# Kernel optimization log

Hardware: AMD Instinct MI355X
Metric: run time of the kernel (lower is better)

The kernel has to match this reference:

```python
import jax, jax.numpy as jnp
import numpy as np

N, IN_DIM, HID, HEADS, HOPS, NCLS, E = 20000, 1536, 256, 4, 3, 3, 320000
HD = HID // HEADS
EPS = 1e-5
NEG_SLOPE = 0.2


def layer_norm(x, g, b):
    mu = jnp.mean(x, axis=-1, keepdims=True)
    var = jnp.var(x, axis=-1, keepdims=True)
    return (x - mu) * jax.lax.rsqrt(var + EPS) * g + b


def gatv2(x, src, dst, Wl, bl, Wr, br, att, bias):
    # x: [N, HID]; src/dst: [E'] (self loops included)
    xl = (x @ Wl + bl).reshape(N, HEADS, HD)  # source transform
    xr = (x @ Wr + br).reshape(N, HEADS, HD)  # target transform
    e = jax.nn.leaky_relu(xl[src] + xr[dst], NEG_SLOPE)          # [E', H, D]
    logits = jnp.einsum('ehd,hd->eh', e, att)                     # [E', H]
    m = jax.ops.segment_max(logits, dst, num_segments=N)         # [N, H]
    ex = jnp.exp(logits - m[dst])
    denom = jax.ops.segment_sum(ex, dst, num_segments=N)
    alpha = ex / denom[dst]                                       # softmax per dst
    msg = xl[src] * alpha[:, :, None]                             # [E', H, D]
    out = jax.ops.segment_sum(msg, dst, num_segments=N)
    return out.reshape(N, HID) + bias


def setup_inputs() -> dict:
    key = jax.random.key(0)
    ks = jax.random.split(key, 20)
    s = lambda k, shp, sc: jax.random.normal(k, shp, jnp.float32) * sc
    return {
        'features': s(ks[0], (N, IN_DIM), 1.0),
        'edge_index': jax.random.randint(ks[1], (2, E), 0, N, jnp.int64),
        'proj_W': s(ks[2], (IN_DIM, HID), 0.02),
        'proj_b': jnp.zeros((HID,), jnp.float32),
        'n0_g': jnp.ones((HID,), jnp.float32),
        'n0_b': jnp.zeros((HID,), jnp.float32),
        'Wl': s(ks[3], (HOPS, HID, HID), 0.05),
        'bl': jnp.zeros((HOPS, HID), jnp.float32),
        'Wr': s(ks[4], (HOPS, HID, HID), 0.05),
        'br': jnp.zeros((HOPS, HID), jnp.float32),
        'att': s(ks[5], (HOPS, HEADS, HD), 0.1),
        'gbias': jnp.zeros((HOPS, HID), jnp.float32),
        'ln_g': jnp.ones((HOPS, HID), jnp.float32),
        'ln_b': jnp.zeros((HOPS, HID), jnp.float32),
        'h1_W': s(ks[6], (HID, HID), 0.05),
        'h1_b': jnp.zeros((HID,), jnp.float32),
        'h2_W': s(ks[7], (HID, NCLS), 0.05),
        'h2_b': jnp.zeros((NCLS,), jnp.float32),
    }


def reference(features, edge_index, proj_W, proj_b, n0_g, n0_b, Wl, bl, Wr, br,
              att, gbias, ln_g, ln_b, h1_W, h1_b, h2_W, h2_b):
    # add self loops (PyG GATv2Conv default)
    loop = jnp.arange(N, dtype=edge_index.dtype)
    src = jnp.concatenate([edge_index[0], loop])
    dst = jnp.concatenate([edge_index[1], loop])

    x = layer_norm(features @ proj_W + proj_b, n0_g, n0_b)
    for h in range(HOPS):
        g = gatv2(x, src, dst, Wl[h], bl[h], Wr[h], br[h], att[h], gbias[h])
        x = layer_norm(g + x, ln_g[h], ln_b[h])
    # head (dropout inactive at eval); torch GELU is exact erf form
    x = jax.nn.gelu(x @ h1_W + h1_b, approximate=False)
    return x @ h2_W + h2_b
```

## Files before the change

### kernel.cpp

```cpp
#include <hip/hip_runtime.h>
#include <hip/hip_bf16.h>
#include <math.h>

#define NN 20000
#define INDIM 1536
#define HID 256
#define NE 320000
#define NEDGE (NE + NN)
#define EPSV 1e-5f
#define NEG 0.2f

typedef unsigned short ushort_b;
typedef unsigned int uint32;
typedef __bf16 bf16x8 __attribute__((ext_vector_type(8)));
typedef float f32x4 __attribute__((ext_vector_type(4)));

#define AS1(p) ((const __attribute__((address_space(1))) void*)(p))
#define AS3(p) ((__attribute__((address_space(3))) void*)(p))

__device__ inline ushort_b f2bf(float x) {
  union { float f; uint32 u; } v; v.f = x;
  uint32 r = v.u + 0x7FFFu + ((v.u >> 16) & 1u);
  return (ushort_b)(r >> 16);
}
__device__ inline float bf2f(ushort_b h) {
  union { uint32 u; float f; } v; v.u = ((uint32)h) << 16;
  return v.f;
}
__device__ inline float u2f(uint32 u) {
  union { uint32 u; float f; } v; v.u = u; return v.f;
}
__device__ inline uint32 cvtpk_bf16(float a, float b) {
  uint32 r;
  asm("v_cvt_pk_bf16_f32 %0, %1, %2" : "=v"(r) : "v"(a), "v"(b));
  return r;
}
__device__ inline float4 ldbf4(const ushort_b* p) {
  ushort4 u = *(const ushort4*)p;
  float4 f;
  f.x = bf2f(u.x); f.y = bf2f(u.y); f.z = bf2f(u.z); f.w = bf2f(u.w);
  return f;
}

template<int OUTMODE>
__global__ __launch_bounds__(256, 3) void gemm_mfma(
    const float* __restrict__ Af,
    const ushort_b* __restrict__ Bt0, const ushort_b* __restrict__ Bt1,
    const float* __restrict__ bias0, const float* __restrict__ bias1,
    void* __restrict__ C0, void* __restrict__ C1,
    int Mstore, int Kloop, int Kstride, int kb0, int kb1)
{
  __shared__ ushort_b Bs[3 * 8192];
  const ushort_b* Bt = blockIdx.z ? Bt1 : Bt0;
  const float* bias  = blockIdx.z ? bias1 : bias0;
  void* Cv           = blockIdx.z ? C1 : C0;
  int kbase          = blockIdx.z ? kb1 : kb0;

  int tid = threadIdx.x;
  int wave = tid >> 6, lane = tid & 63;
  int quad = lane >> 4, mrow = lane & 15;
  int r0 = blockIdx.y * 128;
  int p  = blockIdx.x;
  int nk = Kloop >> 5;
  int nchunk = Kstride >> 5;
  int cb = kbase >> 5;

  int arow0 = r0 + (wave << 5) + mrow;
  int arow1 = arow0 + 16;
  if (arow0 >= Mstore) arow0 = Mstore - 1;
  if (arow1 >= Mstore) arow1 = Mstore - 1;
  const float* Aptr0 = Af + (size_t)arow0 * Kstride + kbase + (quad << 3);
  const float* Aptr1 = Af + (size_t)arow1 * Kstride + kbase + (quad << 3);

  f32x4 acc[2][8] = {};
  float pA0[16], pA1[16];

  auto issueB = [&](int kc, int buf) {
    const char* g = (const char*)Bt + (((size_t)(p * nchunk + (cb + kc))) << 14);
    char* l = (char*)Bs + buf * 16384;
    int o = tid << 4;
#pragma unroll
    for (int pl = 0; pl < 2; pl++) {
      int off = (pl << 13) + o;
      __builtin_amdgcn_global_load_lds(AS1(g + off), AS3(l + off), 16, 0, 0);
      __builtin_amdgcn_global_load_lds(AS1(g + off + 4096), AS3(l + off + 4096), 16, 0, 0);
    }
  };
  auto loadA = [&](int k, float* dst) {
    const float* s0 = Aptr0 + (k << 5);
    const float* s1 = Aptr1 + (k << 5);
    *(float4*)(dst)      = *(const float4*)(s0);
    *(float4*)(dst + 4)  = *(const float4*)(s0 + 4);
    *(float4*)(dst + 8)  = *(const float4*)(s1);
    *(float4*)(dst + 12) = *(const float4*)(s1 + 4);
  };
  auto cvtFrag = [&](const float* s, bf16x8& hh, bf16x8& ll) {
    union { bf16x8 v; uint32 u[4]; } H, L;
#pragma unroll
    for (int q2 = 0; q2 < 4; q2++) {
      float a = s[2 * q2], b = s[2 * q2 + 1];
      uint32 hp = cvtpk_bf16(a, b);
      float fa = u2f(hp << 16);
      float fb = u2f(hp & 0xffff0000u);
      H.u[q2] = hp;
      L.u[q2] = cvtpk_bf16(a - fa, b - fb);
    }
    hh = H.v; ll = L.v;
  };
  auto computeStage = [&](int buf, const bf16x8& ah0, const bf16x8& al0,
                          const bf16x8& ah1, const bf16x8& al1) {
    const ushort_b* bp = Bs + buf * 8192;
#pragma unroll
    for (int u = 0; u < 8; u++) {
      bf16x8 bh = *(const bf16x8*)(bp + (u << 9) + (lane << 3));
      bf16x8 bl = *(const bf16x8*)(bp + 4096 + (u << 9) + (lane << 3));
      acc[0][u] = __builtin_amdgcn_mfma_f32_16x16x32_bf16(ah0, bh, acc[0][u], 0, 0, 0);
      acc[0][u] = __builtin_amdgcn_mfma_f32_16x16x32_bf16(al0, bh, acc[0][u], 0, 0, 0);
      acc[0][u] = __builtin_amdgcn_mfma_f32_16x16x32_bf16(ah0, bl, acc[0][u], 0, 0, 0);
      acc[1][u] = __builtin_amdgcn_mfma_f32_16x16x32_bf16(ah1, bh, acc[1][u], 0, 0, 0);
      acc[1][u] = __builtin_amdgcn_mfma_f32_16x16x32_bf16(al1, bh, acc[1][u], 0, 0, 0);
      acc[1][u] = __builtin_amdgcn_mfma_f32_16x16x32_bf16(ah1, bl, acc[1][u], 0, 0, 0);
    }
  };

  loadA(0, pA0);
  issueB(0, 0);
  issueB(1, 1);
  loadA(1, pA1);
  asm volatile("s_waitcnt vmcnt(8)" ::: "memory");
  __builtin_amdgcn_sched_barrier(0);
  __builtin_amdgcn_s_barrier();
  __builtin_amdgcn_sched_barrier(0);

  int bcur = 0;
  for (int k = 0; k < nk; k += 2) {
    int b1 = bcur + 1; if (b1 >= 3) b1 -= 3;
    int b2 = bcur + 2; if (b2 >= 3) b2 -= 3;

    {
      bf16x8 ah0, al0, ah1, al1;
      cvtFrag(pA0, ah0, al0);
      cvtFrag(pA0 + 8, ah1, al1);
      if (k + 2 < nk) { issueB(k + 2, b2); loadA(k + 2, pA0); }
      computeStage(bcur, ah0, al0, ah1, al1);
      if (k + 2 < nk) { asm volatile("s_waitcnt vmcnt(8)" ::: "memory"); }
      else            { asm volatile("s_waitcnt vmcnt(4)" ::: "memory"); }
      __builtin_amdgcn_sched_barrier(0);
      __builtin_amdgcn_s_barrier();
      __builtin_amdgcn_sched_barrier(0);
    }
    {
      bf16x8 ah0, al0, ah1, al1;
      cvtFrag(pA1, ah0, al0);
      cvtFrag(pA1 + 8, ah1, al1);
      if (k + 3 < nk) { issueB(k + 3, bcur); loadA(k + 3, pA1); }
      computeStage(b1, ah0, al0, ah1, al1);
      if (k + 3 < nk) {
        asm volatile("s_waitcnt vmcnt(8)" ::: "memory");
        __builtin_amdgcn_sched_barrier(0);
        __builtin_amdgcn_s_barrier();
        __builtin_amdgcn_sched_barrier(0);
      }
    }
    bcur = b2;
  }

#pragma unroll
  for (int u = 0; u < 8; u++) {
    int col = (p << 7) + (u << 4) + mrow;
    float bb = bias[col];
#pragma unroll
    for (int t = 0; t < 2; t++) {
#pragma unroll
      for (int r = 0; r < 4; r++) {
        int row = r0 + (wave << 5) + (t << 4) + (quad << 2) + r;
        if (row < Mstore) {
          float v = acc[t][u][r] + bb;
          if (OUTMODE == 3) v = 0.5f * v * (1.f + erff(v * 0.70710678118654752f));
          if (OUTMODE == 2) ((ushort_b*)Cv)[(size_t)row * 256 + col] = f2bf(v);
          else              ((float*)Cv)[(size_t)row * 256 + col] = v;
        }
      }
    }
  }
}

__device__ inline void prep_body(const float* __restrict__ W, int ldw, int nchunk,
                                 ushort_b* __restrict__ out, int c, int p, int tid)
{
  ushort_b* base = out + (((size_t)(p * nchunk + c)) << 13);
#pragma unroll
  for (int g0 = 0; g0 < 2; g0++) {
    int g = tid + (g0 << 8);
    int u = g >> 6, l = g & 63;
    int quad = l >> 4, mrow = l & 15;
    int col = (p << 7) + (u << 4) + mrow;
    int krow = (c << 5) + (quad << 3);
    uint32 hu[4], lu[4];
#pragma unroll
    for (int q2 = 0; q2 < 4; q2++) {
      float a = W[(size_t)(krow + 2 * q2) * ldw + col];
      float b = W[(size_t)(krow + 2 * q2 + 1) * ldw + col];
      ushort_b h0 = f2bf(a), h1 = f2bf(b);
      hu[q2] = (uint32)h0 | ((uint32)h1 << 16);
      lu[q2] = (uint32)f2bf(a - bf2f(h0)) | ((uint32)f2bf(b - bf2f(h1)) << 16);
    }
    *(uint4*)(base + (size_t)g * 8)        = make_uint4(hu[0], hu[1], hu[2], hu[3]);
    *(uint4*)(base + 4096 + (size_t)g * 8) = make_uint4(lu[0], lu[1], lu[2], lu[3]);
  }
}

__global__ __launch_bounds__(256) void prep_frag(
    const float* __restrict__ W, int ldw, int nchunk, ushort_b* __restrict__ out)
{
  prep_body(W, ldw, nchunk, out, blockIdx.x, blockIdx.y, threadIdx.x);
}

__global__ __launch_bounds__(256) void prep_frag7(
    const float* __restrict__ Wl, const float* __restrict__ Wr,
    const float* __restrict__ h1W, ushort_b* __restrict__ dst)
{
  int z = blockIdx.z;
  const float* W = (z < 3) ? Wl + (size_t)z * 65536
                 : (z < 6) ? Wr + (size_t)(z - 3) * 65536
                           : h1W;
  prep_body(W, 256, 8, dst + (size_t)z * 131072, blockIdx.x, blockIdx.y, threadIdx.x);
}

__global__ __launch_bounds__(256) void ln_sum_kernel(
    const float* __restrict__ in0, const float* __restrict__ in1,
    const float* __restrict__ g, const float* __restrict__ b,
    float* __restrict__ out, int n)
{
  int wave = threadIdx.x >> 6, lane = threadIdx.x & 63;
  int row = blockIdx.x * 4 + wave;
  if (row >= n) return;
  int c = lane << 2;
  float4 v = *(const float4*)(in0 + (size_t)row * HID + c);
  float4 v1 = *(const float4*)(in1 + (size_t)row * HID + c);
  v.x += v1.x; v.y += v1.y; v.z += v1.z; v.w += v1.w;
  float s1 = v.x + v.y + v.z + v.w;
  float s2 = v.x * v.x + v.y * v.y + v.z * v.z + v.w * v.w;
#pragma unroll
  for (int m = 1; m < 64; m <<= 1) {
    s1 += __shfl_xor(s1, m, 64);
    s2 += __shfl_xor(s2, m, 64);
  }
  float mu = s1 * (1.f / 256.f);
  float var = s2 * (1.f / 256.f) - mu * mu;
  float rstd = rsqrtf(var + EPSV);
  float4 gv = *(const float4*)(g + c);
  float4 bv = *(const float4*)(b + c);
  float4 o;
  o.x = (v.x - mu) * rstd * gv.x + bv.x;
  o.y = (v.y - mu) * rstd * gv.y + bv.y;
  o.z = (v.z - mu) * rstd * gv.z + bv.z;
  o.w = (v.w - mu) * rstd * gv.w + bv.w;
  *(float4*)(out + (size_t)row * HID + c) = o;
}

__global__ void count_kernel(const int* __restrict__ ei, int* __restrict__ cnt)
{
  int e = blockIdx.x * blockDim.x + threadIdx.x;
  if (e < NEDGE) {
    int d = (e < NE) ? ei[NE + e] : (e - NE);
    atomicAdd(&cnt[d], 1);
  }
}

__global__ __launch_bounds__(1024) void scan_kernel(
    const int* __restrict__ cnt, int* __restrict__ offs, int* __restrict__ cursor)
{
  __shared__ int sums[1024];
  int tid = threadIdx.x;
  const int CH = 20;
  int base = tid * CH;
  int loc[CH];
  int s = 0;
#pragma unroll
  for (int i = 0; i < CH; i++) {
    int idx = base + i;
    int v = (idx < NN) ? cnt[idx] : 0;
    loc[i] = s;
    s += v;
  }
  sums[tid] = s;
  __syncthreads();
  for (int off = 1; off < 1024; off <<= 1) {
    int t = (tid >= off) ? sums[tid - off] : 0;
    __syncthreads();
    sums[tid] += t;
    __syncthreads();
  }
  int pre = (tid == 0) ? 0 : sums[tid - 1];
#pragma unroll
  for (int i = 0; i < CH; i++) {
    int idx = base + i;
    if (idx < NN) { int e = pre + loc[i]; offs[idx] = e; cursor[idx] = e; }
  }
  if (tid == 0) offs[NN] = NEDGE;
}

__global__ void scatter_kernel(const int* __restrict__ ei, int* __restrict__ cursor,
                               int* __restrict__ csr_src)
{
  int e = blockIdx.x * blockDim.x + threadIdx.x;
  if (e < NEDGE) {
    int s, d;
    if (e < NE) { s = ei[e]; d = ei[NE + e]; }
    else { s = e - NE; d = e - NE; }
    int p = atomicAdd(&cursor[d], 1);
    csr_src[p] = s;
  }
}

__device__ inline float edge_logit(float4 xv, float4 xrv, float4 attv) {
  float e0 = xv.x + xrv.x, e1 = xv.y + xrv.y, e2 = xv.z + xrv.z, e3 = xv.w + xrv.w;
  e0 = (e0 > 0.f) ? e0 : NEG * e0;
  e1 = (e1 > 0.f) ? e1 : NEG * e1;
  e2 = (e2 > 0.f) ? e2 : NEG * e2;
  e3 = (e3 > 0.f) ? e3 : NEG * e3;
  float lc = e0 * attv.x + e1 * attv.y + e2 * attv.z + e3 * attv.w;
  lc += __shfl_xor(lc, 1, 16);
  lc += __shfl_xor(lc, 2, 16);
  lc += __shfl_xor(lc, 4, 16);
  lc += __shfl_xor(lc, 8, 16);
  return lc;
}

#define ACCUM(i, lg, xv) {                          \
    float w = __expf(lg);                            \
    lS[i] += w;                                      \
    pS##i##0 += w * xv.x; pS##i##1 += w * xv.y;      \
    pS##i##2 += w * xv.z; pS##i##3 += w * xv.w; }

__global__ __launch_bounds__(256) void gat_kernel(
    const ushort_b* __restrict__ xl, const ushort_b* __restrict__ xr,
    const float* __restrict__ x_in, const float* __restrict__ att,
    const float* __restrict__ gbias, const float* __restrict__ ln_g,
    const float* __restrict__ ln_b, const int* __restrict__ offs,
    const int* __restrict__ csr_src, float* __restrict__ x_out)
{
  __shared__ float gbuf[2][64][5];
  int wave = threadIdx.x >> 6, lane = threadIdx.x & 63;
  int nib = wave >> 1, sub = wave & 1;
  int node = blockIdx.x * 2 + nib;
  int c = lane << 2;
  float4 xrv = ldbf4(xr + (size_t)node * HID + c);
  float4 attv = *(const float4*)(att + c);

  float lS[4] = {0.f, 0.f, 0.f, 0.f};
  float pS00 = 0.f, pS01 = 0.f, pS02 = 0.f, pS03 = 0.f;
  float pS10 = 0.f, pS11 = 0.f, pS12 = 0.f, pS13 = 0.f;
  float pS20 = 0.f, pS21 = 0.f, pS22 = 0.f, pS23 = 0.f;
  float pS30 = 0.f, pS31 = 0.f, pS32 = 0.f, pS33 = 0.f;

  int beg = offs[node], end = offs[node + 1];
  int mid = beg + ((end - beg + 1) >> 1);
  int e  = sub ? mid : beg;
  int e1 = sub ? end : mid;
  for (; e + 3 < e1; e += 4) {
    int s0 = csr_src[e], s1 = csr_src[e + 1], s2 = csr_src[e + 2], s3 = csr_src[e + 3];
    float4 x0v = ldbf4(xl + (size_t)s0 * HID + c);
    float4 x1v = ldbf4(xl + (size_t)s1 * HID + c);
    float4 x2v = ldbf4(xl + (size_t)s2 * HID + c);
    float4 x3v = ldbf4(xl + (size_t)s3 * HID + c);
    float g0 = edge_logit(x0v, xrv, attv);
    float g1 = edge_logit(x1v, xrv, attv);
    float g2 = edge_logit(x2v, xrv, attv);
    float g3 = edge_logit(x3v, xrv, attv);
    ACCUM(0, g0, x0v);
    ACCUM(1, g1, x1v);
    ACCUM(2, g2, x2v);
    ACCUM(3, g3, x3v);
  }
  for (; e < e1; e++) {
    int s0 = csr_src[e];
    float4 x0v = ldbf4(xl + (size_t)s0 * HID + c);
    float g0 = edge_logit(x0v, xrv, attv);
    ACCUM(0, g0, x0v);
  }

  float l  = lS[0] + lS[1] + lS[2] + lS[3];
  float q0 = pS00 + pS10 + pS20 + pS30;
  float q1 = pS01 + pS11 + pS21 + pS31;
  float q2 = pS02 + pS12 + pS22 + pS32;
  float q3 = pS03 + pS13 + pS23 + pS33;

  if (sub) {
    gbuf[nib][lane][0] = l;
    gbuf[nib][lane][1] = q0;
    gbuf[nib][lane][2] = q1;
    gbuf[nib][lane][3] = q2;
    gbuf[nib][lane][4] = q3;
  }
  __syncthreads();
  if (sub) return;

  l  += gbuf[nib][lane][0];
  q0 += gbuf[nib][lane][1];
  q1 += gbuf[nib][lane][2];
  q2 += gbuf[nib][lane][3];
  q3 += gbuf[nib][lane][4];

  float inv = 1.f / l;
  float4 xv = *(const float4*)(x_in + (size_t)node * HID + c);
  float4 gb = *(const float4*)(gbias + c);
  float o0 = q0 * inv + gb.x + xv.x;
  float o1 = q1 * inv + gb.y + xv.y;
  float o2 = q2 * inv + gb.z + xv.z;
  float o3 = q3 * inv + gb.w + xv.w;
  float s1s = o0 + o1 + o2 + o3;
  float s2s = o0 * o0 + o1 * o1 + o2 * o2 + o3 * o3;
#pragma unroll
  for (int mmk = 1; mmk < 64; mmk <<= 1) {
    s1s += __shfl_xor(s1s, mmk, 64);
    s2s += __shfl_xor(s2s, mmk, 64);
  }
  float mu = s1s * (1.f / 256.f);
  float var = s2s * (1.f / 256.f) - mu * mu;
  float rstd = rsqrtf(var + EPSV);
  float4 gv = *(const float4*)(ln_g + c);
  float4 bv = *(const float4*)(ln_b + c);
  float4 o;
  o.x = (o0 - mu) * rstd * gv.x + bv.x;
  o.y = (o1 - mu) * rstd * gv.y + bv.y;
  o.z = (o2 - mu) * rstd * gv.z + bv.z;
  o.w = (o3 - mu) * rstd * gv.w + bv.w;
  *(float4*)(x_out + (size_t)node * HID + c) = o;
}

__global__ __launch_bounds__(256) void head2_kernel(
    const float* __restrict__ t1, const float* __restrict__ W,
    const float* __restrict__ bias, float* __restrict__ out)
{
  int wave = threadIdx.x >> 6, lane = threadIdx.x & 63;
  int row = blockIdx.x * 4 + wave;
  if (row >= NN) return;
  int c = lane << 2;
  float4 v = *(const float4*)(t1 + (size_t)row * HID + c);
  float p0 = 0.f, p1 = 0.f, p2 = 0.f;
#pragma unroll
  for (int j = 0; j < 4; j++) {
    float vj = (&v.x)[j];
    p0 += vj * W[(c + j) * 3 + 0];
    p1 += vj * W[(c + j) * 3 + 1];
    p2 += vj * W[(c + j) * 3 + 2];
  }
#pragma unroll
  for (int mm = 1; mm < 64; mm <<= 1) {
    p0 += __shfl_xor(p0, mm, 64);
    p1 += __shfl_xor(p1, mm, 64);
    p2 += __shfl_xor(p2, mm, 64);
  }
  if (lane == 0) {
    out[(size_t)row * 3 + 0] = p0 + bias[0];
    out[(size_t)row * 3 + 1] = p1 + bias[1];
    out[(size_t)row * 3 + 2] = p2 + bias[2];
  }
}

extern "C" void kernel_launch(void* const* d_in, const int* in_sizes, int n_in,
                              void* d_out, int out_size, void* d_ws, size_t ws_size,
                              hipStream_t stream)
{
  const float* features = (const float*)d_in[0];
  const int*   ei       = (const int*)d_in[1];
  const float* proj_W   = (const float*)d_in[2];
  const float* proj_b   = (const float*)d_in[3];
  const float* n0_g     = (const float*)d_in[4];
  const float* n0_b     = (const float*)d_in[5];
  const float* Wl       = (const float*)d_in[6];
  const float* bl       = (const float*)d_in[7];
  const float* Wr       = (const float*)d_in[8];
  const float* br       = (const float*)d_in[9];
  const float* att      = (const float*)d_in[10];
  const float* gbias    = (const float*)d_in[11];
  const float* ln_g     = (const float*)d_in[12];
  const float* ln_b     = (const float*)d_in[13];
  const float* h1_W     = (const float*)d_in[14];
  const float* h1_b     = (const float*)d_in[15];
  const float* h2_W     = (const float*)d_in[16];
  const float* h2_b     = (const float*)d_in[17];
  float* out = (float*)d_out;

  char* w = (char*)d_ws;
  float*    x0    = (float*)w;    w += (size_t)NN * HID * 4;
  float*    x1    = (float*)w;    w += (size_t)NN * HID * 4;
  float*    part1 = (float*)w;    w += (size_t)NN * HID * 4;
  ushort_b* xlb   = (ushort_b*)w; w += (size_t)NN * HID * 2;
  ushort_b* xrb   = (ushort_b*)w; w += (size_t)NN * HID * 2;
  ushort_b* wtp   = (ushort_b*)w; w += (size_t)2 * HID * INDIM * 2;
  ushort_b* w7    = (ushort_b*)w; w += (size_t)14 * HID * HID * 2;
  float* zbias = (float*)w; w += (size_t)HID * 4;
  int* cnt     = (int*)w;  w += (size_t)NN * 4;
  int* offs    = (int*)w;  w += (size_t)(NN + 1) * 4;
  int* cursor  = (int*)w;  w += (size_t)NN * 4;
  int* csr     = (int*)w;  w += (size_t)NEDGE * 4;

  hipMemsetAsync(cnt, 0, (size_t)NN * 4, stream);
  hipMemsetAsync(zbias, 0, (size_t)HID * 4, stream);
  count_kernel<<<(NEDGE + 255) / 256, 256, 0, stream>>>(ei, cnt);
  scan_kernel<<<1, 1024, 0, stream>>>(cnt, offs, cursor);
  scatter_kernel<<<(NEDGE + 255) / 256, 256, 0, stream>>>(ei, cursor, csr);

  prep_frag<<<dim3(INDIM / 32, 2), 256, 0, stream>>>(proj_W, HID, INDIM / 32, wtp);
  prep_frag7<<<dim3(8, 2, 7), 256, 0, stream>>>(Wl, Wr, h1_W, w7);

  const int MB = (NN + 127) / 128;
  dim3 gsplit(2, MB, 2);
  dim3 gsingle(2, MB, 1);

  gemm_mfma<0><<<gsplit, 256, 0, stream>>>(
      features, wtp, wtp, proj_b, zbias, x1, part1, NN, INDIM / 2, INDIM, 0, INDIM / 2);
  ln_sum_kernel<<<(NN + 3) / 4, 256, 0, stream>>>(x1, part1, n0_g, n0_b, x0, NN);

  float* xcur = x0;
  float* xnxt = x1;
  for (int h = 0; h < 3; h++) {
    gemm_mfma<2><<<gsplit, 256, 0, stream>>>(
        xcur, w7 + (size_t)h * 131072, w7 + (size_t)(3 + h) * 131072,
        bl + h * HID, br + h * HID, xlb, xrb, NN, HID, HID, 0, 0);
    gat_kernel<<<NN / 2, 256, 0, stream>>>(
        xlb, xrb, xcur, att + h * HID, gbias + h * HID,
        ln_g + h * HID, ln_b + h * HID, offs, csr, xnxt);
    float* t = xcur; xcur = xnxt; xnxt = t;
  }

  gemm_mfma<3><<<gsingle, 256, 0, stream>>>(
      xcur, w7 + (size_t)6 * 131072, w7 + (size_t)6 * 131072,
      h1_b, h1_b, part1, part1, NN, HID, HID, 0, 0);
  head2_kernel<<<(NN + 3) / 4, 256, 0, stream>>>(part1, h2_W, h2_b, out);
}
```

Before: 586.0 us.

## Use one wave per node in GAT with software-prefetched edge gathers

The GAT aggregation kernel now assigns one wave per destination node instead of splitting each node's edges across two waves. That removes the shared-memory partial-sum exchange and the block barrier. The edge loop is software pipelined: the next four source rows are gathered while the current four are processed. Tail edges are handled by clamping indices and zeroing their weights, which keeps the loop branch-free but adds redundant loads for short neighbour lists. The cost is less parallelism per node and higher register pressure from the double-buffered loads.

```diff
diff --git a/kernel.cpp b/kernel.cpp
--- a/kernel.cpp
+++ b/kernel.cpp
@@ -37,6 +37,11 @@
 }
 __device__ inline float4 ldbf4(const ushort_b* p) {
   ushort4 u = *(const ushort4*)p;
+  float4 f;
+  f.x = bf2f(u.x); f.y = bf2f(u.y); f.z = bf2f(u.z); f.w = bf2f(u.w);
+  return f;
+}
+__device__ inline float4 us4f(ushort4 u) {
   float4 f;
   f.x = bf2f(u.x); f.y = bf2f(u.y); f.z = bf2f(u.z); f.w = bf2f(u.w);
   return f;
@@ -328,11 +333,10 @@
   return lc;
 }
 
-#define ACCUM(i, lg, xv) {                          \
-    float w = __expf(lg);                            \
-    lS[i] += w;                                      \
-    pS##i##0 += w * xv.x; pS##i##1 += w * xv.y;      \
-    pS##i##2 += w * xv.z; pS##i##3 += w * xv.w; }
+#define ACCUM(i, wt, xv) {                             \
+    lS[i] += wt;                                       \
+    pS##i##0 += wt * xv.x; pS##i##1 += wt * xv.y;      \
+    pS##i##2 += wt * xv.z; pS##i##3 += wt * xv.w; }
 
 __global__ __launch_bounds__(256) void gat_kernel(
     const ushort_b* __restrict__ xl, const ushort_b* __restrict__ xr,
@@ -341,10 +345,8 @@
     const float* __restrict__ ln_b, const int* __restrict__ offs,
     const int* __restrict__ csr_src, float* __restrict__ x_out)
 {
-  __shared__ float gbuf[2][64][5];
   int wave = threadIdx.x >> 6, lane = threadIdx.x & 63;
-  int nib = wave >> 1, sub = wave & 1;
-  int node = blockIdx.x * 2 + nib;
+  int node = blockIdx.x * 4 + wave;
   int c = lane << 2;
   float4 xrv = ldbf4(xr + (size_t)node * HID + c);
   float4 attv = *(const float4*)(att + c);
@@ -355,30 +357,52 @@
   float pS20 = 0.f, pS21 = 0.f, pS22 = 0.f, pS23 = 0.f;
   float pS30 = 0.f, pS31 = 0.f, pS32 = 0.f, pS33 = 0.f;
 
-  int beg = offs[node], end = offs[node + 1];
-  int mid = beg + ((end - beg + 1) >> 1);
-  int e  = sub ? mid : beg;
-  int e1 = sub ? end : mid;
-  for (; e + 3 < e1; e += 4) {
-    int s0 = csr_src[e], s1 = csr_src[e + 1], s2 = csr_src[e + 2], s3 = csr_src[e + 3];
-    float4 x0v = ldbf4(xl + (size_t)s0 * HID + c);
-    float4 x1v = ldbf4(xl + (size_t)s1 * HID + c);
-    float4 x2v = ldbf4(xl + (size_t)s2 * HID + c);
-    float4 x3v = ldbf4(xl + (size_t)s3 * HID + c);
+  int e = offs[node], end = offs[node + 1];
+  int last = end - 1;
+
+  int s1i = e + 1 <= last ? e + 1 : last;
+  int s2i = e + 2 <= last ? e + 2 : last;
+  int s3i = e + 3 <= last ? e + 3 : last;
+  int i0 = csr_src[e], i1 = csr_src[s1i], i2 = csr_src[s2i], i3 = csr_src[s3i];
+  ushort4 a0 = *(const ushort4*)(xl + (size_t)i0 * HID + c);
+  ushort4 a1 = *(const ushort4*)(xl + (size_t)i1 * HID + c);
+  ushort4 a2 = *(const ushort4*)(xl + (size_t)i2 * HID + c);
+  ushort4 a3 = *(const ushort4*)(xl + (size_t)i3 * HID + c);
+
+  for (;;) {
+    int rem = end - e;
+    int en = e + 4;
+    bool more = en < end;
+    ushort4 b0, b1, b2, b3;
+    if (more) {
+      int t1i = en + 1 <= last ? en + 1 : last;
+      int t2i = en + 2 <= last ? en + 2 : last;
+      int t3i = en + 3 <= last ? en + 3 : last;
+      int j0 = csr_src[en], j1 = csr_src[t1i], j2 = csr_src[t2i], j3 = csr_src[t3i];
+      b0 = *(const ushort4*)(xl + (size_t)j0 * HID + c);
+      b1 = *(const ushort4*)(xl + (size_t)j1 * HID + c);
+      b2 = *(const ushort4*)(xl + (size_t)j2 * HID + c);
+      b3 = *(const ushort4*)(xl + (size_t)j3 * HID + c);
+    }
+    float4 x0v = us4f(a0);
+    float4 x1v = us4f(a1);
+    float4 x2v = us4f(a2);
+    float4 x3v = us4f(a3);
     float g0 = edge_logit(x0v, xrv, attv);
     float g1 = edge_logit(x1v, xrv, attv);
     float g2 = edge_logit(x2v, xrv, attv);
     float g3 = edge_logit(x3v, xrv, attv);
-    ACCUM(0, g0, x0v);
-    ACCUM(1, g1, x1v);
-    ACCUM(2, g2, x2v);
-    ACCUM(3, g3, x3v);
-  }
-  for (; e < e1; e++) {
-    int s0 = csr_src[e];
-    float4 x0v = ldbf4(xl + (size_t)s0 * HID + c);
-    float g0 = edge_logit(x0v, xrv, attv);
-    ACCUM(0, g0, x0v);
+    float w0 = __expf(g0);
+    float w1 = (rem > 1) ? __expf(g1) : 0.f;
+    float w2 = (rem > 2) ? __expf(g2) : 0.f;
+    float w3 = (rem > 3) ? __expf(g3) : 0.f;
+    ACCUM(0, w0, x0v);
+    ACCUM(1, w1, x1v);
+    ACCUM(2, w2, x2v);
+    ACCUM(3, w3, x3v);
+    if (!more) break;
+    e = en;
+    a0 = b0; a1 = b1; a2 = b2; a3 = b3;
   }
 
   float l  = lS[0] + lS[1] + lS[2] + lS[3];
@@ -386,22 +410,6 @@
   float q1 = pS01 + pS11 + pS21 + pS31;
   float q2 = pS02 + pS12 + pS22 + pS32;
   float q3 = pS03 + pS13 + pS23 + pS33;
-
-  if (sub) {
-    gbuf[nib][lane][0] = l;
-    gbuf[nib][lane][1] = q0;
-    gbuf[nib][lane][2] = q1;
-    gbuf[nib][lane][3] = q2;
-    gbuf[nib][lane][4] = q3;
-  }
-  __syncthreads();
-  if (sub) return;
-
-  l  += gbuf[nib][lane][0];
-  q0 += gbuf[nib][lane][1];
-  q1 += gbuf[nib][lane][2];
-  q2 += gbuf[nib][lane][3];
-  q3 += gbuf[nib][lane][4];
 
   float inv = 1.f / l;
   float4 xv = *(const float4*)(x_in + (size_t)node * HID + c);
@@ -521,7 +529,7 @@
     gemm_mfma<2><<<gsplit, 256, 0, stream>>>(
         xcur, w7 + (size_t)h * 131072, w7 + (size_t)(3 + h) * 131072,
         bl + h * HID, br + h * HID, xlb, xrb, NN, HID, HID, 0, 0);
-    gat_kernel<<<NN / 2, 256, 0, stream>>>(
+    gat_kernel<<<NN / 4, 256, 0, stream>>>(
         xlb, xrb, xcur, att + h * HID, gbias + h * HID,
         ln_g + h * HID, ln_b + h * HID, offs, csr, xnxt);
     float* t = xcur; xcur = xnxt; xnxt = t;
```

Result: no change. 582.9 us (-0.5%).
